# Performance work log

Hardware: AMD Instinct MI355X
Metric: run time of the kernel (lower is better)

## Reference

```python
import jax, jax.numpy as jnp
from jax import lax
import numpy as np

# --- config (matches init_kwargs / cfgs.CLASS_NUM) ---
CLASS_NUM = 20
CONF_THRESH = 0.01
IOU_THRESH = 0.45
TOP_K = 200
NMS_MAX = 400
IMG_W = 300.0  # note: original code uses img_width for BOTH axes (bug replicated)
BATCH, N_BOXES = 64, 8732
LAST = 3 * CLASS_NUM + 5  # 65


def setup_inputs() -> dict:
    key = jax.random.key(0)
    y_pred = jax.random.uniform(key, (BATCH, N_BOXES, LAST), dtype=jnp.float32)
    return {"y_pred": y_pred}


def _iou_one_vs_many(box, boxes):
    # box: [4] (xmin,ymin,xmax,ymax); boxes: [M,4]
    x1 = jnp.maximum(box[0], boxes[:, 0])
    y1 = jnp.maximum(box[1], boxes[:, 1])
    x2 = jnp.minimum(box[2], boxes[:, 2])
    y2 = jnp.minimum(box[3], boxes[:, 3])
    inter = jnp.maximum(x2 - x1, 0.0) * jnp.maximum(y2 - y1, 0.0)
    area_a = jnp.maximum(box[2] - box[0], 0.0) * jnp.maximum(box[3] - box[1], 0.0)
    area_b = jnp.maximum(boxes[:, 2] - boxes[:, 0], 0.0) * jnp.maximum(boxes[:, 3] - boxes[:, 1], 0.0)
    union = area_a + area_b - inter
    return jnp.where(union > 0.0, inter / jnp.maximum(union, 1e-8), 0.0)


def _nms_item(preds):
    # preds: [N, 6] rows = [class_id, conf, xmin, ymin, xmax, ymax]
    conf = preds[:, 1]
    valid = conf > CONF_THRESH  # confidence thresholding (class_id != -1 is always true)
    # sort: valid boxes first, by descending confidence
    order = jnp.argsort(jnp.where(valid, -conf, jnp.inf))
    sp = preds[order]            # [N,6]
    sv = valid[order]            # [N]

    def step(state, inp):
        sel_pred, sel_mask, count = state  # [M,6], [M] float, int32
        p, v = inp
        ious = _iou_one_vs_many(p[2:6], sel_pred[:, 2:6]) * sel_mask
        keep = v & (count < NMS_MAX) & (jnp.max(ious) <= IOU_THRESH)
        w = jnp.minimum(count, NMS_MAX - 1)
        new_row = jnp.where(keep, p, sel_pred[w])
        sel_pred = sel_pred.at[w].set(new_row)
        sel_mask = sel_mask.at[w].set(jnp.where(keep, 1.0, sel_mask[w]))
        count = count + keep.astype(jnp.int32)
        return (sel_pred, sel_mask, count), None

    init = (jnp.zeros((NMS_MAX, 6), jnp.float32), jnp.zeros((NMS_MAX,), jnp.float32), jnp.int32(0))
    (sel_pred, sel_mask, _), _ = lax.scan(step, init, (sp, sv))
    sel_pred = sel_pred * sel_mask[:, None]  # zero-pad unselected slots
    # top_k by confidence, sorted descending (NMS_MAX >= TOP_K so always enough rows)
    _, top_idx = lax.top_k(sel_pred[:, 1], TOP_K)
    return sel_pred[top_idx]  # [TOP_K, 6]


def _forward(y_pred):
    C = CLASS_NUM
    # clip boxes to image boundary; original buggily uses img_width for both axes
    coords = jnp.clip(y_pred[..., -4:], 0.0, IMG_W - 1.0)  # [B,N,4] xmin,ymin,xmax,ymax
    probs = y_pred[..., C:2 * C] * y_pred[..., 2 * C + 1:-4]  # [B,N,C]
    class_ids = (jnp.argmax(probs, axis=-1) + 1).astype(jnp.float32)[..., None]
    confidences = jnp.max(probs, axis=-1, keepdims=True)
    preds = jnp.concatenate([class_ids, confidences, coords], axis=-1)  # [B,N,6]
    return jax.vmap(_nms_item)(preds)  # [B, TOP_K, 6]


def reference(y_pred):
    return _forward(y_pred)
```

## Files before the change

### kernel.cpp

```cpp
#include <hip/hip_runtime.h>
#include <cstdint>
#include <cstddef>

using u64 = unsigned long long;

namespace {
constexpr int kClassNum = 20;
constexpr int kBatch    = 64;
constexpr int kNBoxes   = 8732;
constexpr int kLast     = 65;
constexpr int kTopK     = 200;
constexpr int kNmsCap   = 200;
constexpr int kHist     = 1024;
constexpr int kSelM     = 384;
constexpr int kCand     = 512;
constexpr float kPreT   = 0.9f;
constexpr int kB09      = 0x3F66 - 0x3C23;
constexpr int kFThreads = 1024;
constexpr int kConfThreads = 256;
constexpr int kRows     = 128;
constexpr int kRBlocks  = (kNBoxes + kRows - 1) / kRows;
constexpr int kSlots    = 32;
constexpr int kPoolW    = kRBlocks * kSlots;
constexpr int kNIter    = (kNBoxes + kFThreads - 1) / kFThreads;
constexpr int kPWIter   = (kPoolW + kFThreads - 1) / kFThreads;
constexpr int kGroups   = kCand / 64;
}

__device__ __forceinline__ int bucket_of_key(u64 k) {
  int b = (int)(unsigned)(k >> 48) - 0x3C23;
  return min(max(b, 0), kHist - 1);
}

__device__ __forceinline__ float iou_f(float a0, float a1, float a2, float a3,
                                       float areaA, float4 bb) {
  const float ix1 = fmaxf(a0, bb.x);
  const float iy1 = fmaxf(a1, bb.y);
  const float ix2 = fminf(a2, bb.z);
  const float iy2 = fminf(a3, bb.w);
  const float inter = fmaxf(ix2 - ix1, 0.0f) * fmaxf(iy2 - iy1, 0.0f);
  const float areaB = fmaxf(bb.z - bb.x, 0.0f) * fmaxf(bb.w - bb.y, 0.0f);
  const float un = areaA + areaB - inter;
  return (un > 0.0f) ? inter / fmaxf(un, 1e-8f) : 0.0f;
}

__device__ __forceinline__ u64 readlane64(u64 x, int l) {
  const unsigned lo = (unsigned)__builtin_amdgcn_readlane((int)(unsigned)x, l);
  const unsigned hi = (unsigned)__builtin_amdgcn_readlane((int)(unsigned)(x >> 32), l);
  return ((u64)hi << 32) | (u64)lo;
}

__global__ __launch_bounds__(kConfThreads) void conf_kernel(const float* __restrict__ y,
                                                            float* __restrict__ confs,
                                                            u64* __restrict__ pool,
                                                            int* __restrict__ bcnt) {
  __shared__ float tile[kRows * kLast];
  __shared__ int wcnt[kConfThreads / 64];
  const int item = blockIdx.y;
  const int blk  = blockIdx.x;
  const int base = blk * kRows;
  const int nb   = min(kRows, kNBoxes - base);
  const int tid  = threadIdx.x;
  const int lane = tid & 63;
  const int wv   = tid >> 6;

  const float4* src4 = (const float4*)(y + ((size_t)item * kNBoxes + base) * kLast);
  float4* t4 = (float4*)tile;
  const int nf4 = nb * kLast / 4;
  for (int k = tid; k < nf4; k += kConfThreads) t4[k] = src4[k];
  __syncthreads();

  float conf = 0.0f;
  if (tid < nb) {
    const float* row = tile + tid * kLast;
    float best = row[20] * row[41];
#pragma unroll
    for (int c = 1; c < kClassNum; ++c) best = fmaxf(best, row[20 + c] * row[41 + c]);
    conf = best;
    confs[(size_t)item * kNBoxes + base + tid] = best;
  }

  const bool take = conf > kPreT;
  const u64 bal = __ballot(take);
  if (lane == 0) wcnt[wv] = __popcll(bal);
  __syncthreads();
  int pre = 0, total = 0;
#pragma unroll
  for (int w = 0; w < kConfThreads / 64; ++w) {
    const int c = wcnt[w];
    if (w < wv) pre += c;
    total += c;
  }
  u64* pblk = pool + (size_t)item * kPoolW + blk * kSlots;
  if (take) {
    const int rank = pre + __popcll(bal & ((1ull << lane) - 1ull));
    if (rank < kSlots)
      pblk[rank] = ((u64)__float_as_uint(conf) << 32) |
                   (u64)(0xFFFFFFFFu - (unsigned)(base + tid));
  }
  if (tid < kSlots && tid >= total) pblk[tid] = 0;
  if (tid == 0) bcnt[item * kRBlocks + blk] = total;
}

__device__ __forceinline__ u64 shfl_xor_u64(u64 x, int d) {
  int lo = __shfl_xor((int)(unsigned)x, d, 64);
  int hi = __shfl_xor((int)(unsigned)(x >> 32), d, 64);
  return ((u64)(unsigned)hi << 32) | (u64)(unsigned)lo;
}

__device__ __forceinline__ u64 cmpsel(u64 a, u64 b, bool keepmax) {
  u64 mx = a > b ? a : b;
  u64 mn = a > b ? b : a;
  return keepmax ? mx : mn;
}

template <int J, int K>
__device__ __forceinline__ void stage1(u64& k, int i, bool act, u64* buf) {
  if constexpr (J >= 64) {
    __syncthreads();
    if (act) buf[i] = k;
    __syncthreads();
    if (act) {
      const u64 pv = buf[i ^ J];
      const bool lower = (i & J) == 0;
      const bool desc  = (i & K) == 0;
      k = cmpsel(k, pv, desc == lower);
    }
  } else {
    const u64 pv = shfl_xor_u64(k, J);
    const bool lower = (i & J) == 0;
    const bool desc  = (i & K) == 0;
    k = cmpsel(k, pv, desc == lower);
  }
}

template <int K, int J>
__device__ __forceinline__ void cascade1(u64& k, int i, bool act, u64* buf) {
  stage1<J, K>(k, i, act, buf);
  if constexpr (J > 1) cascade1<K, (J >> 1)>(k, i, act, buf);
}

__global__ __launch_bounds__(kFThreads) void fused_kernel(const float* __restrict__ y,
                                                          const float* __restrict__ confs,
                                                          const u64* __restrict__ pool,
                                                          const int* __restrict__ bcnt,
                                                          float* __restrict__ out) {
  __shared__ u64    buf[kCand];
  __shared__ int    hist[kHist];
  __shared__ int    wtot[16];
  __shared__ int    tails[16];
  __shared__ float4 selbox[kNmsCap];
  __shared__ float2 selmeta[kNmsCap];
  __shared__ float4 selact[kNmsCap];
  __shared__ float4 candbox[2][64];
  __shared__ float  candcls[2][64];
  __shared__ float  candconf[2][64];
  __shared__ u64    g_validm[2];
  __shared__ u64    supB[16];
  __shared__ u64    colm[64];
  __shared__ int g_cnt, g_count, g_active, g_done, g_thr, g_bad;

  const int item = blockIdx.x;
  const int tid  = threadIdx.x;
  const int lane = tid & 63;
  const int wv   = tid >> 6;
  const float* cbase = confs + (size_t)item * kNBoxes;
  const u64* pbase = pool + (size_t)item * kPoolW;
  const float* ybase = y + (size_t)item * kNBoxes * kLast;

  hist[tid] = 0;
  if (tid == 0) { g_cnt = 0; g_count = 0; g_active = 0; g_done = 0; g_thr = 0; g_bad = 0; }
  __syncthreads();
  if (tid < kRBlocks && bcnt[item * kRBlocks + tid] > kSlots) g_bad = 1;
  __syncthreads();
  const bool pooled = (g_bad == 0);

  u64 kv[kNIter];
  auto load_fallback = [&]() {
#pragma unroll
    for (int r = 0; r < kNIter; ++r) {
      const int i = tid + r * kFThreads;
      const float c = (i < kNBoxes) ? cbase[i] : 0.0f;
      kv[r] = (c > 0.01f)
                  ? (((u64)__float_as_uint(c) << 32) | (u64)(0xFFFFFFFFu - (unsigned)i))
                  : 0ull;
    }
  };
  auto build_hist = [&]() {
#pragma unroll
    for (int r = 0; r < kNIter; ++r)
      if (kv[r]) atomicAdd(&hist[bucket_of_key(kv[r])], 1);
    __syncthreads();
  };
  auto suffix_scan = [&]() {
    int v = hist[tid];
#pragma unroll
    for (int off = 1; off < 64; off <<= 1) {
      const int o = __shfl_down(v, off, 64);
      if (lane + off < 64) v += o;
    }
    if (lane == 0) wtot[wv] = v;
    __syncthreads();
    if (tid < 16) {
      int t = wtot[tid];
#pragma unroll
      for (int off = 1; off < 16; off <<= 1) {
        const int o = __shfl_down(t, off, 64);
        if (tid + off < 16) t += o;
      }
      tails[tid] = t - wtot[tid];
    }
    __syncthreads();
    hist[tid] = v + tails[wv];
    __syncthreads();
  };

  if (pooled) {
#pragma unroll
    for (int r = 0; r < kNIter; ++r) {
      const int i = tid + r * kFThreads;
      kv[r] = (r < kPWIter && i < kPoolW) ? pbase[i] : 0ull;
    }
  } else {
    load_fallback();
  }
  build_hist();
  suffix_scan();

  if (pooled && hist[kB09 + 1] < kSelM) {
    hist[tid] = 0;
    __syncthreads();
    load_fallback();
    build_hist();
    suffix_scan();
  }

  {
    const int S  = hist[tid];
    const int Sn = (tid < kHist - 1) ? hist[tid + 1] : 0;
    if (S >= kSelM && Sn < kSelM) g_thr = tid;
  }
  __syncthreads();
  const int T0 = g_thr;
  const int T  = (hist[T0] > kCand && T0 < kHist - 1) ? T0 + 1 : T0;

#pragma unroll
  for (int r = 0; r < kNIter; ++r) {
    const bool take = kv[r] && (bucket_of_key(kv[r]) >= T);
    const u64 bal = __ballot(take);
    int wbase = 0;
    if (lane == 0 && bal) wbase = atomicAdd(&g_cnt, __popcll(bal));
    wbase = __shfl(wbase, 0, 64);
    if (take) {
      const int pos = wbase + __popcll(bal & ((1ull << lane) - 1ull));
      if (pos < kCand) buf[pos] = kv[r];
    }
  }
  __syncthreads();
  const int ncand = min(g_cnt, kCand);
  for (int i2 = ncand + tid; i2 < kCand; i2 += kFThreads) buf[i2] = 0;
  __syncthreads();

  {
    const bool act = tid < kCand;
    u64 k = act ? buf[tid] : 0ull;
    cascade1<2, 1>(k, tid, act, buf);
    cascade1<4, 2>(k, tid, act, buf);
    cascade1<8, 4>(k, tid, act, buf);
    cascade1<16, 8>(k, tid, act, buf);
    cascade1<32, 16>(k, tid, act, buf);
    cascade1<64, 32>(k, tid, act, buf);
    cascade1<128, 64>(k, tid, act, buf);
    cascade1<256, 128>(k, tid, act, buf);
    cascade1<512, 256>(k, tid, act, buf);
    __syncthreads();
    if (act) buf[tid] = k;
  }
  __syncthreads();

  auto gather = [&](int g, int slot) {
    float4 box = make_float4(0.f, 0.f, 0.f, 0.f);
    float cls = 0.f, cf = 0.f;
    int val = 0;
    if (g < kGroups) {
      const u64 key = buf[g * 64 + lane];
      if (key >> 32) {
        val = 1;
        cf = __uint_as_float((unsigned)(key >> 32));
        const unsigned idx = 0xFFFFFFFFu - (unsigned)key;
        const float* row = ybase + (size_t)idx * kLast;
        float best = row[20] * row[41];
        int cl = 1;
#pragma unroll
        for (int c = 1; c < kClassNum; ++c) {
          const float p = row[20 + c] * row[41 + c];
          if (p > best) { best = p; cl = c + 1; }
        }
        cls = (float)cl;
        const float c0 = fminf(fmaxf(row[61], 0.0f), 299.0f);
        const float c1 = fminf(fmaxf(row[62], 0.0f), 299.0f);
        const float c2 = fminf(fmaxf(row[63], 0.0f), 299.0f);
        const float c3 = fminf(fmaxf(row[64], 0.0f), 299.0f);
        box = make_float4(c0, c1, c2, c3);
      }
    }
    candbox[slot][lane]  = box;
    candcls[slot][lane]  = cls;
    candconf[slot][lane] = cf;
    const u64 vm = __ballot(val);
    if (lane == 0) g_validm[slot] = vm;
  };

  if (wv == 0) gather(0, 0);
  __syncthreads();

  int cur = 0;
  for (int g = 0; g < kGroups; ++g) {
    const int count = g_count;
    const int act   = g_active;

    const float4 bx = candbox[cur][lane];
    const float a0 = bx.x, a1 = bx.y, a2 = bx.z, a3 = bx.w;
    const float areaA = fmaxf(a2 - a0, 0.0f) * fmaxf(a3 - a1, 0.0f);
    float m = 0.0f;
    if (areaA > 0.0f) {
      for (int s = wv; s < act; s += 16) m = fmaxf(m, iou_f(a0, a1, a2, a3, areaA, selact[s]));
    }
    {
      const u64 pb = __ballot(m > 0.45f);
      if (lane == 0) supB[wv] = pb;
    }

#pragma unroll
    for (int jj = 0; jj < 4; ++jj) {
      const int j = wv * 4 + jj;
      const float4 bb = candbox[cur][j];
      const float areaB = fmaxf(bb.z - bb.x, 0.0f) * fmaxf(bb.w - bb.y, 0.0f);
      u64 cm = 0ull;
      if (areaB > 0.0f) {
        const float iou = iou_f(a0, a1, a2, a3, areaA, bb);
        cm = __ballot((j < lane) && (iou > 0.45f));
      }
      if (lane == 0) colm[j] = cm;
    }
    __syncthreads();

    if (wv == 1) gather(g + 1, cur ^ 1);
    if (wv == 0) {
      u64 supm = 0ull;
#pragma unroll
      for (int ww = 0; ww < 16; ++ww) supm |= supB[ww];
      const u64 mycol  = colm[lane];
      const u64 validm = g_validm[cur];

      u64 avail = validm & ~supm;
      u64 keptm = 0ull;
      int cnt2 = count;
      int done = 0;
      while (avail) {
        const int j = __builtin_ctzll(avail);
        keptm |= (1ull << j);
        if (++cnt2 >= kNmsCap) { done = 1; break; }
        const u64 cj = readlane64(mycol, j);
        avail &= ~(cj | (1ull << j));
      }
      if (validm != ~0ull) done = 1;

      const u64 below = (1ull << lane) - 1ull;
      const u64 actm = keptm & __ballot(areaA > 0.0f);
      if ((keptm >> lane) & 1ull) {
        const int wdx = count + __popcll(keptm & below);
        if (wdx < kNmsCap) {
          selbox[wdx]  = bx;
          selmeta[wdx] = make_float2(candcls[cur][lane], candconf[cur][lane]);
        }
      }
      if ((actm >> lane) & 1ull) {
        const int adx = act + __popcll(actm & below);
        if (adx < kNmsCap) selact[adx] = bx;
      }
      if (lane == 0) {
        g_count  = min(cnt2, kNmsCap);
        g_active = min(act + __popcll(actm), kNmsCap);
        g_done   = done;
      }
    }
    __syncthreads();
    if (g_done) break;
    cur ^= 1;
  }

  const int count = g_count;
  float* obase = out + (size_t)item * kTopK * 6;
  for (int slot = tid; slot < kTopK; slot += kFThreads) {
    float* o = obase + (size_t)slot * 6;
    if (slot < count) {
      const float4 bsel = selbox[slot];
      const float2 mta  = selmeta[slot];
      o[0] = mta.x; o[1] = mta.y; o[2] = bsel.x; o[3] = bsel.y; o[4] = bsel.z; o[5] = bsel.w;
    } else {
      o[0] = 0.0f; o[1] = 0.0f; o[2] = 0.0f; o[3] = 0.0f; o[4] = 0.0f; o[5] = 0.0f;
    }
  }
}

extern "C" void kernel_launch(void* const* d_in, const int* in_sizes, int n_in,
                              void* d_out, int out_size, void* d_ws, size_t ws_size,
                              hipStream_t stream) {
  const float* y = (const float*)d_in[0];
  float* out = (float*)d_out;

  float* confs = (float*)d_ws;
  u64* pool = (u64*)(confs + (size_t)kBatch * kNBoxes);
  int* bcnt = (int*)(pool + (size_t)kBatch * kPoolW);

  dim3 cgrid(kRBlocks, kBatch);
  conf_kernel<<<cgrid, kConfThreads, 0, stream>>>(y, confs, pool, bcnt);
  fused_kernel<<<kBatch, kFThreads, 0, stream>>>(y, confs, pool, bcnt, out);
}
```

Measured before the change: 66.35 us.

## Halve fused block to 512 threads, coarsen histogram, gather all candidates upfront

Reduces the fused NMS block from 1024 to 512 threads and halves the histogram to 512 buckets by shifting keys one more bit. Keys are no longer held in registers; they are streamed from global memory twice, once for the histogram and once for the append. All 512 candidates' rows are gathered in parallel up front instead of one group at a time overlapped with NMS. The aim is to use fewer threads and registers and simplify the pipeline, at the cost of re-reading the inputs and a coarser threshold selection.

```diff
diff --git a/kernel.cpp b/kernel.cpp
--- a/kernel.cpp
+++ b/kernel.cpp
@@ -11,24 +11,28 @@
 constexpr int kLast     = 65;
 constexpr int kTopK     = 200;
 constexpr int kNmsCap   = 200;
-constexpr int kHist     = 1024;
+constexpr int kHist     = 512;
 constexpr int kSelM     = 384;
 constexpr int kCand     = 512;
 constexpr float kPreT   = 0.9f;
-constexpr int kB09      = 0x3F66 - 0x3C23;
-constexpr int kFThreads = 1024;
+constexpr int kB09      = 0x1FB3 - 0x1E11;
+constexpr int kFThreads = 512;
 constexpr int kConfThreads = 256;
 constexpr int kRows     = 128;
 constexpr int kRBlocks  = (kNBoxes + kRows - 1) / kRows;
 constexpr int kSlots    = 32;
 constexpr int kPoolW    = kRBlocks * kSlots;
-constexpr int kNIter    = (kNBoxes + kFThreads - 1) / kFThreads;
-constexpr int kPWIter   = (kPoolW + kFThreads - 1) / kFThreads;
+constexpr int kPIterP   = (kPoolW + kFThreads - 1) / kFThreads;
+constexpr int kPIterF   = (kNBoxes + kFThreads - 1) / kFThreads;
 constexpr int kGroups   = kCand / 64;
 }
 
 __device__ __forceinline__ int bucket_of_key(u64 k) {
-  int b = (int)(unsigned)(k >> 48) - 0x3C23;
+  int b = (int)(unsigned)(k >> 49) - 0x1E11;
+  return min(max(b, 0), kHist - 1);
+}
+__device__ __forceinline__ int bucket_of_conf(float c) {
+  int b = (int)(__float_as_uint(c) >> 17) - 0x1E11;
   return min(max(b, 0), kHist - 1);
 }
 
@@ -115,17 +119,15 @@
 }
 
 template <int J, int K>
-__device__ __forceinline__ void stage1(u64& k, int i, bool act, u64* buf) {
+__device__ __forceinline__ void stage1(u64& k, int i, u64* buf) {
   if constexpr (J >= 64) {
     __syncthreads();
-    if (act) buf[i] = k;
-    __syncthreads();
-    if (act) {
-      const u64 pv = buf[i ^ J];
-      const bool lower = (i & J) == 0;
-      const bool desc  = (i & K) == 0;
-      k = cmpsel(k, pv, desc == lower);
-    }
+    buf[i] = k;
+    __syncthreads();
+    const u64 pv = buf[i ^ J];
+    const bool lower = (i & J) == 0;
+    const bool desc  = (i & K) == 0;
+    k = cmpsel(k, pv, desc == lower);
   } else {
     const u64 pv = shfl_xor_u64(k, J);
     const bool lower = (i & J) == 0;
@@ -135,9 +137,9 @@
 }
 
 template <int K, int J>
-__device__ __forceinline__ void cascade1(u64& k, int i, bool act, u64* buf) {
-  stage1<J, K>(k, i, act, buf);
-  if constexpr (J > 1) cascade1<K, (J >> 1)>(k, i, act, buf);
+__device__ __forceinline__ void cascade1(u64& k, int i, u64* buf) {
+  stage1<J, K>(k, i, buf);
+  if constexpr (J > 1) cascade1<K, (J >> 1)>(k, i, buf);
 }
 
 __global__ __launch_bounds__(kFThreads) void fused_kernel(const float* __restrict__ y,
@@ -147,16 +149,16 @@
                                                           float* __restrict__ out) {
   __shared__ u64    buf[kCand];
   __shared__ int    hist[kHist];
-  __shared__ int    wtot[16];
-  __shared__ int    tails[16];
+  __shared__ int    wtot[8];
+  __shared__ int    tails[8];
   __shared__ float4 selbox[kNmsCap];
   __shared__ float2 selmeta[kNmsCap];
   __shared__ float4 selact[kNmsCap];
-  __shared__ float4 candbox[2][64];
-  __shared__ float  candcls[2][64];
-  __shared__ float  candconf[2][64];
-  __shared__ u64    g_validm[2];
-  __shared__ u64    supB[16];
+  __shared__ float4 cbox[kCand];
+  __shared__ float  ccls[kCand];
+  __shared__ float  cconf[kCand];
+  __shared__ u64    gvalidm[kGroups];
+  __shared__ u64    supB[8];
   __shared__ u64    colm[64];
   __shared__ int g_cnt, g_count, g_active, g_done, g_thr, g_bad;
 
@@ -173,23 +175,27 @@
   __syncthreads();
   if (tid < kRBlocks && bcnt[item * kRBlocks + tid] > kSlots) g_bad = 1;
   __syncthreads();
-  const bool pooled = (g_bad == 0);
-
-  u64 kv[kNIter];
-  auto load_fallback = [&]() {
-#pragma unroll
-    for (int r = 0; r < kNIter; ++r) {
-      const int i = tid + r * kFThreads;
-      const float c = (i < kNBoxes) ? cbase[i] : 0.0f;
-      kv[r] = (c > 0.01f)
-                  ? (((u64)__float_as_uint(c) << 32) | (u64)(0xFFFFFFFFu - (unsigned)i))
-                  : 0ull;
-    }
-  };
-  auto build_hist = [&]() {
-#pragma unroll
-    for (int r = 0; r < kNIter; ++r)
-      if (kv[r]) atomicAdd(&hist[bucket_of_key(kv[r])], 1);
+  bool full = (g_bad != 0);
+
+  auto build_hist = [&](bool fullsrc) {
+    if (!fullsrc) {
+#pragma unroll
+      for (int r = 0; r < kPIterP; ++r) {
+        const int i = tid + r * kFThreads;
+        if (i < kPoolW) {
+          const u64 k = pbase[i];
+          if (k) atomicAdd(&hist[bucket_of_key(k)], 1);
+        }
+      }
+    } else {
+      for (int r = 0; r < kPIterF; ++r) {
+        const int i = tid + r * kFThreads;
+        if (i < kNBoxes) {
+          const float c = cbase[i];
+          if (c > 0.01f) atomicAdd(&hist[bucket_of_conf(c)], 1);
+        }
+      }
+    }
     __syncthreads();
   };
   auto suffix_scan = [&]() {
@@ -201,12 +207,12 @@
     }
     if (lane == 0) wtot[wv] = v;
     __syncthreads();
-    if (tid < 16) {
+    if (tid < 8) {
       int t = wtot[tid];
 #pragma unroll
-      for (int off = 1; off < 16; off <<= 1) {
+      for (int off = 1; off < 8; off <<= 1) {
         const int o = __shfl_down(t, off, 64);
-        if (tid + off < 16) t += o;
+        if (tid + off < 8) t += o;
       }
       tails[tid] = t - wtot[tid];
     }
@@ -215,23 +221,13 @@
     __syncthreads();
   };
 
-  if (pooled) {
-#pragma unroll
-    for (int r = 0; r < kNIter; ++r) {
-      const int i = tid + r * kFThreads;
-      kv[r] = (r < kPWIter && i < kPoolW) ? pbase[i] : 0ull;
-    }
-  } else {
-    load_fallback();
-  }
-  build_hist();
+  build_hist(full);
   suffix_scan();
-
-  if (pooled && hist[kB09 + 1] < kSelM) {
+  if (!full && hist[kB09 + 1] < kSelM) {
     hist[tid] = 0;
     __syncthreads();
-    load_fallback();
-    build_hist();
+    full = true;
+    build_hist(true);
     suffix_scan();
   }
 
@@ -244,16 +240,33 @@
   const int T0 = g_thr;
   const int T  = (hist[T0] > kCand && T0 < kHist - 1) ? T0 + 1 : T0;
 
-#pragma unroll
-  for (int r = 0; r < kNIter; ++r) {
-    const bool take = kv[r] && (bucket_of_key(kv[r]) >= T);
+  auto append = [&](u64 k) {
+    const bool take = k && (bucket_of_key(k) >= T);
     const u64 bal = __ballot(take);
     int wbase = 0;
     if (lane == 0 && bal) wbase = atomicAdd(&g_cnt, __popcll(bal));
     wbase = __shfl(wbase, 0, 64);
     if (take) {
       const int pos = wbase + __popcll(bal & ((1ull << lane) - 1ull));
-      if (pos < kCand) buf[pos] = kv[r];
+      if (pos < kCand) buf[pos] = k;
+    }
+  };
+  if (!full) {
+#pragma unroll
+    for (int r = 0; r < kPIterP; ++r) {
+      const int i = tid + r * kFThreads;
+      append((i < kPoolW) ? pbase[i] : 0ull);
+    }
+  } else {
+    for (int r = 0; r < kPIterF; ++r) {
+      const int i = tid + r * kFThreads;
+      u64 k = 0ull;
+      if (i < kNBoxes) {
+        const float c = cbase[i];
+        if (c > 0.01f)
+          k = ((u64)__float_as_uint(c) << 32) | (u64)(0xFFFFFFFFu - (unsigned)i);
+      }
+      append(k);
     }
   }
   __syncthreads();
@@ -262,69 +275,63 @@
   __syncthreads();
 
   {
-    const bool act = tid < kCand;
-    u64 k = act ? buf[tid] : 0ull;
-    cascade1<2, 1>(k, tid, act, buf);
-    cascade1<4, 2>(k, tid, act, buf);
-    cascade1<8, 4>(k, tid, act, buf);
-    cascade1<16, 8>(k, tid, act, buf);
-    cascade1<32, 16>(k, tid, act, buf);
-    cascade1<64, 32>(k, tid, act, buf);
-    cascade1<128, 64>(k, tid, act, buf);
-    cascade1<256, 128>(k, tid, act, buf);
-    cascade1<512, 256>(k, tid, act, buf);
-    __syncthreads();
-    if (act) buf[tid] = k;
-  }
-  __syncthreads();
-
-  auto gather = [&](int g, int slot) {
+    u64 k = buf[tid];
+    cascade1<2, 1>(k, tid, buf);
+    cascade1<4, 2>(k, tid, buf);
+    cascade1<8, 4>(k, tid, buf);
+    cascade1<16, 8>(k, tid, buf);
+    cascade1<32, 16>(k, tid, buf);
+    cascade1<64, 32>(k, tid, buf);
+    cascade1<128, 64>(k, tid, buf);
+    cascade1<256, 128>(k, tid, buf);
+    cascade1<512, 256>(k, tid, buf);
+    __syncthreads();
+    buf[tid] = k;
+  }
+  __syncthreads();
+
+  {
+    const u64 key = buf[tid];
     float4 box = make_float4(0.f, 0.f, 0.f, 0.f);
     float cls = 0.f, cf = 0.f;
     int val = 0;
-    if (g < kGroups) {
-      const u64 key = buf[g * 64 + lane];
-      if (key >> 32) {
-        val = 1;
-        cf = __uint_as_float((unsigned)(key >> 32));
-        const unsigned idx = 0xFFFFFFFFu - (unsigned)key;
-        const float* row = ybase + (size_t)idx * kLast;
-        float best = row[20] * row[41];
-        int cl = 1;
-#pragma unroll
-        for (int c = 1; c < kClassNum; ++c) {
-          const float p = row[20 + c] * row[41 + c];
-          if (p > best) { best = p; cl = c + 1; }
-        }
-        cls = (float)cl;
-        const float c0 = fminf(fmaxf(row[61], 0.0f), 299.0f);
-        const float c1 = fminf(fmaxf(row[62], 0.0f), 299.0f);
-        const float c2 = fminf(fmaxf(row[63], 0.0f), 299.0f);
-        const float c3 = fminf(fmaxf(row[64], 0.0f), 299.0f);
-        box = make_float4(c0, c1, c2, c3);
-      }
-    }
-    candbox[slot][lane]  = box;
-    candcls[slot][lane]  = cls;
-    candconf[slot][lane] = cf;
+    if (key >> 32) {
+      val = 1;
+      cf = __uint_as_float((unsigned)(key >> 32));
+      const unsigned idx = 0xFFFFFFFFu - (unsigned)key;
+      const float* row = ybase + (size_t)idx * kLast;
+      float best = row[20] * row[41];
+      int cl = 1;
+#pragma unroll
+      for (int c = 1; c < kClassNum; ++c) {
+        const float p = row[20 + c] * row[41 + c];
+        if (p > best) { best = p; cl = c + 1; }
+      }
+      cls = (float)cl;
+      const float c0 = fminf(fmaxf(row[61], 0.0f), 299.0f);
+      const float c1 = fminf(fmaxf(row[62], 0.0f), 299.0f);
+      const float c2 = fminf(fmaxf(row[63], 0.0f), 299.0f);
+      const float c3 = fminf(fmaxf(row[64], 0.0f), 299.0f);
+      box = make_float4(c0, c1, c2, c3);
+    }
+    cbox[tid]  = box;
+    ccls[tid]  = cls;
+    cconf[tid] = cf;
     const u64 vm = __ballot(val);
-    if (lane == 0) g_validm[slot] = vm;
-  };
-
-  if (wv == 0) gather(0, 0);
-  __syncthreads();
-
-  int cur = 0;
+    if (lane == 0) gvalidm[wv] = vm;
+  }
+  __syncthreads();
+
   for (int g = 0; g < kGroups; ++g) {
     const int count = g_count;
     const int act   = g_active;
 
-    const float4 bx = candbox[cur][lane];
+    const float4 bx = cbox[g * 64 + lane];
     const float a0 = bx.x, a1 = bx.y, a2 = bx.z, a3 = bx.w;
     const float areaA = fmaxf(a2 - a0, 0.0f) * fmaxf(a3 - a1, 0.0f);
     float m = 0.0f;
     if (areaA > 0.0f) {
-      for (int s = wv; s < act; s += 16) m = fmaxf(m, iou_f(a0, a1, a2, a3, areaA, selact[s]));
+      for (int s = wv; s < act; s += 8) m = fmaxf(m, iou_f(a0, a1, a2, a3, areaA, selact[s]));
     }
     {
       const u64 pb = __ballot(m > 0.45f);
@@ -332,9 +339,9 @@
     }
 
 #pragma unroll
-    for (int jj = 0; jj < 4; ++jj) {
-      const int j = wv * 4 + jj;
-      const float4 bb = candbox[cur][j];
+    for (int jj = 0; jj < 8; ++jj) {
+      const int j = wv * 8 + jj;
+      const float4 bb = cbox[g * 64 + j];
       const float areaB = fmaxf(bb.z - bb.x, 0.0f) * fmaxf(bb.w - bb.y, 0.0f);
       u64 cm = 0ull;
       if (areaB > 0.0f) {
@@ -345,13 +352,12 @@
     }
     __syncthreads();
 
-    if (wv == 1) gather(g + 1, cur ^ 1);
     if (wv == 0) {
       u64 supm = 0ull;
 #pragma unroll
-      for (int ww = 0; ww < 16; ++ww) supm |= supB[ww];
+      for (int ww = 0; ww < 8; ++ww) supm |= supB[ww];
       const u64 mycol  = colm[lane];
-      const u64 validm = g_validm[cur];
+      const u64 validm = gvalidm[g];
 
       u64 avail = validm & ~supm;
       u64 keptm = 0ull;
@@ -372,7 +378,7 @@
         const int wdx = count + __popcll(keptm & below);
         if (wdx < kNmsCap) {
           selbox[wdx]  = bx;
-          selmeta[wdx] = make_float2(candcls[cur][lane], candconf[cur][lane]);
+          selmeta[wdx] = make_float2(ccls[g * 64 + lane], cconf[g * 64 + lane]);
         }
       }
       if ((actm >> lane) & 1ull) {
@@ -387,7 +393,6 @@
     }
     __syncthreads();
     if (g_done) break;
-    cur ^= 1;
   }
 
   const int count = g_count;
```

After: 69.24 us. 4.4% more time.
